# Kernel optimization log

Measured on AMD Instinct MI355X. Metric: run time of the kernel, lower is better.

Reference implementation:

```python
import jax, jax.numpy as jnp
import numpy as np

B, D, N = 4096, 4096, 4  # batch, feature dim, number of branches


def setup_inputs() -> dict:
    key = jax.random.key(0)
    k0, k1, k2, k3, kg = jax.random.split(key, 5)
    return {
        "branch0": jax.random.normal(k0, (B, D), dtype=jnp.float32),
        "branch1": jax.random.normal(k1, (B, D), dtype=jnp.float32),
        "branch2": jax.random.normal(k2, (B, D), dtype=jnp.float32),
        "branch3": jax.random.normal(k3, (B, D), dtype=jnp.float32),
        "gate": jax.random.normal(kg, (B, N), dtype=jnp.float32),
    }


def reference(branch0, branch1, branch2, branch3, gate):
    # Stack branches: [N, B, D]
    branches = jnp.stack([branch0, branch1, branch2, branch3], axis=0)
    n = branches.shape[0]
    # inner_predict: argmax over gate logits, then one-hot encode -> [B, N]
    onehot = jax.nn.one_hot(jnp.argmax(gate, axis=1), n, dtype=branches.dtype)
    # Per-sample weighted sum over branches (equivalent to the TensorArray loop)
    return jnp.einsum("nbd,bn->bd", branches, onehot)
```

## Files before the change

### kernel.cpp

```cpp
#include <hip/hip_runtime.h>
#include <hip/hip_bf16.h>


#define B 4096
#define D 4096

__global__ __launch_bounds__(256) void combine_kernel(
    const float* __restrict__ b0, const float* __restrict__ b1,
    const float* __restrict__ b2, const float* __restrict__ b3,
    const float* __restrict__ gate, float* __restrict__ out) {

    const int row = blockIdx.x;

    float4 g = ((const float4*)gate)[row];

    int idx = 0;
    float best = g.x;
    if (g.y > best) { best = g.y; idx = 1; }
    if (g.z > best) { best = g.z; idx = 2; }
    if (g.w > best) { best = g.w; idx = 3; }

    const float* src = (idx == 0) ? b0 : (idx == 1) ? b1 : (idx == 2) ? b2 : b3;

    const float4* s = (const float4*)(src + (size_t)row * D);
    float4*       d = (float4*)(out + (size_t)row * D);

    #pragma unroll
    for (int k = 0; k < 4; ++k) {
        int c = threadIdx.x + k * 256;
        d[c] = s[c];
    }
}

extern "C" void kernel_launch(void* const* d_in, const int* in_sizes, int n_in,
                              void* d_out, int out_size, void* d_ws, size_t ws_size,
                              hipStream_t stream) {
    const float* b0   = (const float*)d_in[0];
    const float* b1   = (const float*)d_in[1];
    const float* b2   = (const float*)d_in[2];
    const float* b3   = (const float*)d_in[3];
    const float* gate = (const float*)d_in[4];
    float* out = (float*)d_out;

    combine_kernel<<<B, 256, 0, stream>>>(b0, b1, b2, b3, gate, out);
}
```

Measured before the change: 216.4 us.

## Process four rows per block with interleaved loads and nontemporal stores

Each block now handles four rows instead of one. It computes all four gate argmaxes up front, then interleaves row loads and stores so several rows of loads are in flight at once. Output writes use nontemporal stores to avoid polluting the cache. The cost is more registers per thread and four times fewer blocks, which could reduce occupancy or the spread of work across CUs.

```diff
diff --git a/kernel.cpp b/kernel.cpp
--- a/kernel.cpp
+++ b/kernel.cpp
@@ -1,35 +1,69 @@
 #include <hip/hip_runtime.h>
-#include <hip/hip_bf16.h>
 
 
 #define B 4096
 #define D 4096
+#define ROWS 4
+#define NBLK (B / ROWS)
+
+typedef float f32x4 __attribute__((ext_vector_type(4)));
 
 __global__ __launch_bounds__(256) void combine_kernel(
     const float* __restrict__ b0, const float* __restrict__ b1,
     const float* __restrict__ b2, const float* __restrict__ b3,
     const float* __restrict__ gate, float* __restrict__ out) {
 
-    const int row = blockIdx.x;
+    const int t = threadIdx.x;
+    const int row0 = blockIdx.x * ROWS;
 
-    float4 g = ((const float4*)gate)[row];
+    const f32x4* src[ROWS];
+    f32x4* dst[ROWS];
+    #pragma unroll
+    for (int r = 0; r < ROWS; ++r) {
+        const int row = row0 + r;
+        f32x4 g = ((const f32x4*)gate)[row];
+        int idx = 0;
+        float best = g.x;
+        if (g.y > best) { best = g.y; idx = 1; }
+        if (g.z > best) { best = g.z; idx = 2; }
+        if (g.w > best) { best = g.w; idx = 3; }
+        const float* p = (idx == 0) ? b0 : (idx == 1) ? b1 : (idx == 2) ? b2 : b3;
+        src[r] = (const f32x4*)(p + (size_t)row * D);
+        dst[r] = (f32x4*)(out + (size_t)row * D);
+    }
 
-    int idx = 0;
-    float best = g.x;
-    if (g.y > best) { best = g.y; idx = 1; }
-    if (g.z > best) { best = g.z; idx = 2; }
-    if (g.w > best) { best = g.w; idx = 3; }
+    f32x4 a0, a1, a2, a3;
+    f32x4 c0, c1, c2, c3;
+    f32x4 e0, e1, e2, e3;
+    f32x4 h0, h1, h2, h3;
 
-    const float* src = (idx == 0) ? b0 : (idx == 1) ? b1 : (idx == 2) ? b2 : b3;
+#define LOADROW(v0, v1, v2, v3, r)                                          \
+    do {                                                                    \
+        const f32x4* s_ = src[r];                                           \
+        v0 = s_[t];       v1 = s_[t + 256];                                 \
+        v2 = s_[t + 512]; v3 = s_[t + 768];                                 \
+    } while (0)
 
-    const float4* s = (const float4*)(src + (size_t)row * D);
-    float4*       d = (float4*)(out + (size_t)row * D);
+#define STOREROW(v0, v1, v2, v3, r)                                         \
+    do {                                                                    \
+        f32x4* d_ = dst[r];                                                 \
+        __builtin_nontemporal_store(v0, &d_[t]);                            \
+        __builtin_nontemporal_store(v1, &d_[t + 256]);                      \
+        __builtin_nontemporal_store(v2, &d_[t + 512]);                      \
+        __builtin_nontemporal_store(v3, &d_[t + 768]);                      \
+    } while (0)
 
-    #pragma unroll
-    for (int k = 0; k < 4; ++k) {
-        int c = threadIdx.x + k * 256;
-        d[c] = s[c];
-    }
+    LOADROW(a0, a1, a2, a3, 0);
+    LOADROW(c0, c1, c2, c3, 1);
+    STOREROW(a0, a1, a2, a3, 0);
+    LOADROW(e0, e1, e2, e3, 2);
+    STOREROW(c0, c1, c2, c3, 1);
+    LOADROW(h0, h1, h2, h3, 3);
+    STOREROW(e0, e1, e2, e3, 2);
+    STOREROW(h0, h1, h2, h3, 3);
+
+#undef LOADROW
+#undef STOREROW
 }
 
 extern "C" void kernel_launch(void* const* d_in, const int* in_sizes, int n_in,
@@ -42,5 +76,5 @@
     const float* gate = (const float*)d_in[4];
     float* out = (float*)d_out;
 
-    combine_kernel<<<B, 256, 0, stream>>>(b0, b1, b2, b3, gate, out);
+    combine_kernel<<<NBLK, 256, 0, stream>>>(b0, b1, b2, b3, gate, out);
 }
```

New measurement: 218.8 us. No clear change (+1.1%).
